# Kernel optimization log

Measured on AMD Instinct MI355X. Metric: run time of the kernel, lower is better.

## Reference

```python
import math
import jax, jax.numpy as jnp
import numpy as np

HALF_PI = math.pi / 2
TWOR_SCALE = 1.0 / math.log(2.0)
B, C, L, K = 32, 2, 262144, 4


def setup_inputs() -> dict:
    key = jax.random.key(0)
    ks = jax.random.split(key, 6)
    return {
        "input_signal": jax.random.normal(ks[0], (B, C, L), jnp.float32),
        "twoR": jax.random.normal(ks[1], (B, K), jnp.float32),
        "G": jax.random.normal(ks[2], (B, K), jnp.float32),
        "c_hp": jax.random.normal(ks[3], (B, K), jnp.float32),
        "c_bp": jax.random.normal(ks[4], (B, K), jnp.float32),
        "c_lp": jax.random.normal(ks[5], (B, K), jnp.float32),
    }


def get_biquad_coefficients(twoR, G, c_hp, c_bp, c_lp):
    # each arg: (B, K)
    G2 = G * G
    b0 = c_hp + c_bp * G + c_lp * G2
    b1 = -2.0 * c_hp + 2.0 * c_lp * G2
    b2 = c_hp - c_bp * G + c_lp * G2
    a0 = 1.0 + G2 + twoR * G
    a1 = 2.0 * G2 - 2.0
    a2 = 1.0 + G2 - twoR * G
    return jnp.stack([b0, b1, b2], -1), jnp.stack([a0, a1, a2], -1)  # (B,K,3)


def _biquad_cascade(x, Bs, As):
    # x: (B,C,L); Bs, As: (B,1,K,3) -- broadcast over channels.
    # Direct-form II transposed, cascaded in series over K filters.
    Bs = Bs / As[..., :1]
    As = As / As[..., :1]
    b_, c_ = x.shape[0], x.shape[1]
    y = x
    num_filters = Bs.shape[2]
    for k in range(num_filters):
        b0, b1, b2 = Bs[:, :, k, 0], Bs[:, :, k, 1], Bs[:, :, k, 2]  # (B,1)
        a1, a2 = As[:, :, k, 1], As[:, :, k, 2]  # (B,1)

        def step(carry, xt):
            s1, s2 = carry
            yt = b0 * xt + s1              # (B,C)
            s1n = b1 * xt - a1 * yt + s2
            s2n = b2 * xt - a2 * yt
            return (s1n, s2n), yt

        init = (jnp.zeros((b_, c_), y.dtype), jnp.zeros((b_, c_), y.dtype))
        _, yT = jax.lax.scan(step, init, jnp.moveaxis(y, -1, 0))  # (L,B,C)
        y = jnp.moveaxis(yT, 0, -1)
    return y


def reference(input_signal, twoR, G, c_hp, c_bp, c_lp):
    G = jnp.tan(HALF_PI * jax.nn.sigmoid(G))
    twoR = TWOR_SCALE * jax.nn.softplus(twoR) + 0.01
    Bs, As = get_biquad_coefficients(twoR, G, c_hp, c_bp, c_lp)  # (B,K,3)
    Bs, As = Bs[:, None], As[:, None]  # unsqueeze(1): (B,1,K,3)
    return _biquad_cascade(input_signal, Bs, As)
```

## Files before the change

### kernel.cpp

```cpp
#include <hip/hip_runtime.h>
#include <math.h>

#define B_N 32
#define C_N 2
#define L_N 262144
#define K_N 4
#define NSEQ (B_N * C_N)
#define CHUNK 32
#define THREADS 256
#define BLKSAMP (CHUNK * THREADS)
#define NBLK_SEQ (L_N / BLKSAMP)
#define NBLK_TOT (NSEQ * NBLK_SEQ)
#define NLVL 8
#define ROWW 33

#define WS_COEF 0
#define WS_PL   (B_N * 20)
#define WS_PBLK (WS_PL + B_N * NLVL * 64)
#define WS_AGG  (WS_PBLK + B_N * 64)

__global__ __launch_bounds__(64) void svf_prep(
    const float* __restrict__ twoR, const float* __restrict__ Graw,
    const float* __restrict__ c_hp, const float* __restrict__ c_bp,
    const float* __restrict__ c_lp, float* __restrict__ ws)
{
    const int b = blockIdx.x;
    const int t = threadIdx.x;
    __shared__ double cf[K_N][5];
    __shared__ double M[8][8];

    if (t < K_N) {
        const int k = t;
        double g  = (double)Graw[b * K_N + k];
        double tr = (double)twoR[b * K_N + k];
        double hp = (double)c_hp[b * K_N + k];
        double bp = (double)c_bp[b * K_N + k];
        double lp = (double)c_lp[b * K_N + k];
        double sg = 1.0 / (1.0 + exp(-g));
        double G  = tan(1.5707963267948966 * sg);
        double R  = log1p(exp(tr)) * 1.4426950408889634 + 0.01;
        double G2 = G * G;
        double b0 = hp + bp * G + lp * G2;
        double b1 = -2.0 * hp + 2.0 * lp * G2;
        double b2 = hp - bp * G + lp * G2;
        double a0 = 1.0 + G2 + R * G;
        double a1 = 2.0 * G2 - 2.0;
        double a2 = 1.0 + G2 - R * G;
        cf[k][0] = b0 / a0; cf[k][1] = b1 / a0; cf[k][2] = b2 / a0;
        cf[k][3] = a1 / a0; cf[k][4] = a2 / a0;
    }
    __syncthreads();

    if (t < 20) ws[WS_COEF + b * 20 + t] = (float)cf[t / 5][t % 5];

    if (t < 8) {
        double s[8];
        #pragma unroll
        for (int i = 0; i < 8; ++i) s[i] = (i == t) ? 1.0 : 0.0;
        double in = 0.0;
        #pragma unroll
        for (int k = 0; k < K_N; ++k) {
            double y   = cf[k][0] * in + s[2 * k];
            double s1n = cf[k][1] * in - cf[k][3] * y + s[2 * k + 1];
            double s2n = cf[k][2] * in - cf[k][4] * y;
            s[2 * k] = s1n; s[2 * k + 1] = s2n; in = y;
        }
        #pragma unroll
        for (int i = 0; i < 8; ++i) M[i][t] = s[i];
    }
    __syncthreads();

    const int i = t >> 3, j = t & 7;
    for (int p = 1; p <= 13; ++p) {
        double acc = 0.0;
        #pragma unroll
        for (int k = 0; k < 8; ++k) acc += M[i][k] * M[k][j];
        __syncthreads();
        M[i][j] = acc;
        __syncthreads();
        if (p >= 5 && p <= 12) ws[WS_PL + (b * NLVL + (p - 5)) * 64 + t] = (float)acc;
        if (p == 13)           ws[WS_PBLK + b * 64 + t] = (float)acc;
    }
}

__device__ __forceinline__ float cascade_step(const float cf[20], float s[8], float in)
{
    #pragma unroll
    for (int k = 0; k < K_N; ++k) {
        float y  = fmaf(cf[k * 5 + 0], in, s[2 * k]);
        float t1 = fmaf(cf[k * 5 + 1], in, s[2 * k + 1]);
        float n1 = fmaf(-cf[k * 5 + 3], y, t1);
        float n2 = fmaf(-cf[k * 5 + 4], y, cf[k * 5 + 2] * in);
        s[2 * k] = n1; s[2 * k + 1] = n2;
        in = y;
    }
    return in;
}

__device__ __forceinline__ void stage_load(const float4* __restrict__ xg4,
                                           float* __restrict__ win,
                                           float* __restrict__ xr, int tid)
{
    float4 v4[8];
    #pragma unroll
    for (int j = 0; j < 8; ++j) v4[j] = xg4[tid + j * THREADS];
    const int myw = tid >> 6, lane = tid & 63;
    #pragma unroll
    for (int r = 0; r < 4; ++r) {
        #pragma unroll
        for (int h = 0; h < 2; ++h) {
            const int fw = tid + h * THREADS;
            const int a  = (fw >> 3) * ROWW + (fw & 7) * 4;
            float4 v = v4[2 * r + h];
            win[a] = v.x; win[a + 1] = v.y; win[a + 2] = v.z; win[a + 3] = v.w;
        }
        __syncthreads();
        if (myw == r) {
            #pragma unroll
            for (int j = 0; j < CHUNK; ++j) xr[j] = win[lane * ROWW + j];
        }
        __syncthreads();
    }
}

__global__ __launch_bounds__(THREADS) void svf_pass1(
    const float* __restrict__ x, const float* __restrict__ ws,
    float* __restrict__ out)
{
    const int seq = blockIdx.x >> 5;
    const int blk = blockIdx.x & (NBLK_SEQ - 1);
    const int tid = threadIdx.x;
    const int b   = seq >> 1;

    __shared__ float smem[THREADS * 9];
    __shared__ float Pm[NLVL * 64];

    for (int q = tid; q < NLVL * 64; q += THREADS)
        Pm[q] = ws[WS_PL + b * NLVL * 64 + q];

    float cf[20];
    #pragma unroll
    for (int q = 0; q < 20; ++q) cf[q] = ws[WS_COEF + b * 20 + q];

    const size_t base = (size_t)seq * L_N + (size_t)blk * BLKSAMP;
    float xr[CHUNK];
    stage_load((const float4*)(x + base), smem, xr, tid);

    float t[8] = {0, 0, 0, 0, 0, 0, 0, 0};
    #pragma unroll
    for (int j = 0; j < CHUNK; ++j) (void)cascade_step(cf, t, xr[j]);

    for (int l = 0; l < NLVL; ++l) {
        const int d = 1 << l;
        #pragma unroll
        for (int q = 0; q < 8; ++q) smem[tid * 9 + q] = t[q];
        __syncthreads();
        float prev[8];
        const bool have = (tid >= d);
        if (have) {
            #pragma unroll
            for (int q = 0; q < 8; ++q) prev[q] = smem[(tid - d) * 9 + q];
        }
        __syncthreads();
        if (have) {
            #pragma unroll
            for (int r = 0; r < 8; ++r) {
                float acc = t[r];
                #pragma unroll
                for (int c = 0; c < 8; ++c)
                    acc = fmaf(Pm[l * 64 + r * 8 + c], prev[c], acc);
                t[r] = acc;
            }
        }
    }
    #pragma unroll
    for (int q = 0; q < 8; ++q) smem[tid * 9 + q] = t[q];
    __syncthreads();

    float e[8] = {0, 0, 0, 0, 0, 0, 0, 0};
    if (tid > 0) {
        #pragma unroll
        for (int q = 0; q < 8; ++q) e[q] = smem[(tid - 1) * 9 + q];
    }
    float4* eo = (float4*)(out + base);
    eo[2 * tid]     = make_float4(e[0], e[1], e[2], e[3]);
    eo[2 * tid + 1] = make_float4(e[4], e[5], e[6], e[7]);

    if (tid == THREADS - 1) {
        float* agg = (float*)ws + WS_AGG + (size_t)blockIdx.x * 8;
        #pragma unroll
        for (int q = 0; q < 8; ++q) agg[q] = t[q];
    }
}

__global__ __launch_bounds__(64) void svf_scanb(float* __restrict__ ws)
{
    const int seq = threadIdx.x;
    const int b   = seq >> 1;
    float P[64];
    #pragma unroll
    for (int q = 0; q < 64; ++q) P[q] = ws[WS_PBLK + b * 64 + q];

    float* agg = ws + WS_AGG + (size_t)seq * NBLK_SEQ * 8;

    float t[8] = {0, 0, 0, 0, 0, 0, 0, 0};
    for (int j = 0; j < NBLK_SEQ; ++j) {
        float f[8];
        #pragma unroll
        for (int q = 0; q < 8; ++q) f[q] = agg[j * 8 + q];
        #pragma unroll
        for (int q = 0; q < 8; ++q) agg[j * 8 + q] = t[q];
        float nt[8];
        #pragma unroll
        for (int r = 0; r < 8; ++r) {
            float acc = f[r];
            #pragma unroll
            for (int c = 0; c < 8; ++c) acc = fmaf(P[r * 8 + c], t[c], acc);
            nt[r] = acc;
        }
        #pragma unroll
        for (int q = 0; q < 8; ++q) t[q] = nt[q];
    }
}

__global__ __launch_bounds__(THREADS) void svf_pass2(
    const float* __restrict__ x, const float* __restrict__ ws,
    float* __restrict__ out)
{
    const int seq = blockIdx.x >> 5;
    const int blk = blockIdx.x & (NBLK_SEQ - 1);
    const int tid = threadIdx.x;
    const int b   = seq >> 1;

    __shared__ float smem[THREADS * 9];
    __shared__ float Pm[NLVL * 64];

    const size_t base = (size_t)seq * L_N + (size_t)blk * BLKSAMP;

    const float4* eo = (const float4*)(out + base);
    float4 e0 = eo[2 * tid], e1 = eo[2 * tid + 1];

    const float* sbp = ws + WS_AGG + (size_t)blockIdx.x * 8;
    float v[8];
    #pragma unroll
    for (int q = 0; q < 8; ++q) v[q] = sbp[q];

    for (int q = tid; q < NLVL * 64; q += THREADS)
        Pm[q] = ws[WS_PL + b * NLVL * 64 + q];

    float cf[20];
    #pragma unroll
    for (int q = 0; q < 20; ++q) cf[q] = ws[WS_COEF + b * 20 + q];

    float xr[CHUNK];
    stage_load((const float4*)(x + base), smem, xr, tid);

    #pragma unroll
    for (int l = 0; l < NLVL; ++l) {
        if ((tid >> l) & 1) {
            float nv[8];
            #pragma unroll
            for (int r = 0; r < 8; ++r) {
                float acc = 0.0f;
                #pragma unroll
                for (int c = 0; c < 8; ++c)
                    acc = fmaf(Pm[l * 64 + r * 8 + c], v[c], acc);
                nv[r] = acc;
            }
            #pragma unroll
            for (int q = 0; q < 8; ++q) v[q] = nv[q];
        }
    }

    float s[8] = {e0.x + v[0], e0.y + v[1], e0.z + v[2], e0.w + v[3],
                  e1.x + v[4], e1.y + v[5], e1.z + v[6], e1.w + v[7]};

    #pragma unroll
    for (int j = 0; j < CHUNK; ++j) xr[j] = cascade_step(cf, s, xr[j]);

    const int myw = tid >> 6, lane = tid & 63;
    float4* og4 = (float4*)(out + base);
    for (int r = 0; r < 4; ++r) {
        if (myw == r) {
            #pragma unroll
            for (int j = 0; j < CHUNK; ++j) smem[lane * ROWW + j] = xr[j];
        }
        __syncthreads();
        #pragma unroll
        for (int h = 0; h < 2; ++h) {
            const int fw = tid + h * THREADS;
            const int a  = (fw >> 3) * ROWW + (fw & 7) * 4;
            og4[r * 512 + fw] =
                make_float4(smem[a], smem[a + 1], smem[a + 2], smem[a + 3]);
        }
        __syncthreads();
    }
}

extern "C" void kernel_launch(void* const* d_in, const int* in_sizes, int n_in,
                              void* d_out, int out_size, void* d_ws, size_t ws_size,
                              hipStream_t stream)
{
    (void)in_sizes; (void)n_in; (void)out_size; (void)ws_size;
    const float* x    = (const float*)d_in[0];
    const float* twoR = (const float*)d_in[1];
    const float* G    = (const float*)d_in[2];
    const float* chp  = (const float*)d_in[3];
    const float* cbp  = (const float*)d_in[4];
    const float* clp  = (const float*)d_in[5];
    float* out = (float*)d_out;
    float* ws  = (float*)d_ws;

    svf_prep <<<B_N, 64, 0, stream>>>(twoR, G, chp, cbp, clp, ws);
    svf_pass1<<<NBLK_TOT, THREADS, 0, stream>>>(x, ws, out);
    svf_scanb<<<1, 64, 0, stream>>>(ws);
    svf_pass2<<<NBLK_TOT, THREADS, 0, stream>>>(x, ws, out);
}
```

Baseline: 163.9 us.

## Fuse two-pass scan into single kernel with decoupled lookback over flags

```diff
diff --git a/kernel.cpp b/kernel.cpp
--- a/kernel.cpp
+++ b/kernel.cpp
@@ -13,11 +13,12 @@
 #define NBLK_TOT (NSEQ * NBLK_SEQ)
 #define NLVL 8
 #define ROWW 33
+#define FLAG_READY 0x1F2E3D4Cu
 
 #define WS_COEF 0
 #define WS_PL   (B_N * 20)
-#define WS_PBLK (WS_PL + B_N * NLVL * 64)
-#define WS_AGG  (WS_PBLK + B_N * 64)
+#define WS_AGG  (WS_PL + B_N * NLVL * 64)
+#define WS_FLAG (WS_AGG + NBLK_TOT * 8)
 
 __global__ __launch_bounds__(64) void svf_prep(
     const float* __restrict__ twoR, const float* __restrict__ Graw,
@@ -26,6 +27,9 @@
 {
     const int b = blockIdx.x;
     const int t = threadIdx.x;
+
+    ((unsigned*)(ws + WS_FLAG))[b * 64 + t] = 0u;
+
     __shared__ double cf[K_N][5];
     __shared__ double M[8][8];
 
@@ -71,15 +75,14 @@
     __syncthreads();
 
     const int i = t >> 3, j = t & 7;
-    for (int p = 1; p <= 13; ++p) {
+    for (int p = 1; p <= 12; ++p) {
         double acc = 0.0;
         #pragma unroll
         for (int k = 0; k < 8; ++k) acc += M[i][k] * M[k][j];
         __syncthreads();
         M[i][j] = acc;
         __syncthreads();
-        if (p >= 5 && p <= 12) ws[WS_PL + (b * NLVL + (p - 5)) * 64 + t] = (float)acc;
-        if (p == 13)           ws[WS_PBLK + b * 64 + t] = (float)acc;
+        if (p >= 5) ws[WS_PL + (b * NLVL + (p - 5)) * 64 + t] = (float)acc;
     }
 }
 
@@ -97,14 +100,34 @@
     return in;
 }
 
-__device__ __forceinline__ void stage_load(const float4* __restrict__ xg4,
-                                           float* __restrict__ win,
-                                           float* __restrict__ xr, int tid)
-{
+__global__ __launch_bounds__(THREADS, 4) void svf_fused(
+    const float* __restrict__ x, float* __restrict__ ws, float* __restrict__ out)
+{
+    const int seq  = blockIdx.x >> 5;
+    const int blk  = blockIdx.x & (NBLK_SEQ - 1);
+    const int tid  = threadIdx.x;
+    const int b    = seq >> 1;
+    const int myw  = tid >> 6, lane = tid & 63;
+
+    __shared__ float smem[THREADS * 9];
+    __shared__ float Pm[NLVL * 64];
+    __shared__ float Pb[64];
+    __shared__ float fl[NBLK_SEQ][8];
+    __shared__ float sbv[8];
+
+    for (int q = tid; q < NLVL * 64; q += THREADS)
+        Pm[q] = ws[WS_PL + b * NLVL * 64 + q];
+
+    float cf[20];
+    #pragma unroll
+    for (int q = 0; q < 20; ++q) cf[q] = ws[WS_COEF + b * 20 + q];
+
+    const size_t base = (size_t)seq * L_N + (size_t)blk * BLKSAMP;
+    const float4* xg4 = (const float4*)(x + base);
     float4 v4[8];
     #pragma unroll
     for (int j = 0; j < 8; ++j) v4[j] = xg4[tid + j * THREADS];
-    const int myw = tid >> 6, lane = tid & 63;
+    float xr[CHUNK];
     #pragma unroll
     for (int r = 0; r < 4; ++r) {
         #pragma unroll
@@ -112,39 +135,24 @@
             const int fw = tid + h * THREADS;
             const int a  = (fw >> 3) * ROWW + (fw & 7) * 4;
             float4 v = v4[2 * r + h];
-            win[a] = v.x; win[a + 1] = v.y; win[a + 2] = v.z; win[a + 3] = v.w;
+            smem[a] = v.x; smem[a + 1] = v.y; smem[a + 2] = v.z; smem[a + 3] = v.w;
         }
         __syncthreads();
         if (myw == r) {
             #pragma unroll
-            for (int j = 0; j < CHUNK; ++j) xr[j] = win[lane * ROWW + j];
-        }
-        __syncthreads();
-    }
-}
-
-__global__ __launch_bounds__(THREADS) void svf_pass1(
-    const float* __restrict__ x, const float* __restrict__ ws,
-    float* __restrict__ out)
-{
-    const int seq = blockIdx.x >> 5;
-    const int blk = blockIdx.x & (NBLK_SEQ - 1);
-    const int tid = threadIdx.x;
-    const int b   = seq >> 1;
-
-    __shared__ float smem[THREADS * 9];
-    __shared__ float Pm[NLVL * 64];
-
-    for (int q = tid; q < NLVL * 64; q += THREADS)
-        Pm[q] = ws[WS_PL + b * NLVL * 64 + q];
-
-    float cf[20];
-    #pragma unroll
-    for (int q = 0; q < 20; ++q) cf[q] = ws[WS_COEF + b * 20 + q];
-
-    const size_t base = (size_t)seq * L_N + (size_t)blk * BLKSAMP;
-    float xr[CHUNK];
-    stage_load((const float4*)(x + base), smem, xr, tid);
+            for (int j = 0; j < CHUNK; ++j) xr[j] = smem[lane * ROWW + j];
+        }
+        __syncthreads();
+    }
+
+    if (tid < 64) {
+        const int r8 = tid >> 3, c8 = tid & 7;
+        float acc = 0.0f;
+        #pragma unroll
+        for (int k = 0; k < 8; ++k)
+            acc = fmaf(Pm[7 * 64 + r8 * 8 + k], Pm[7 * 64 + k * 8 + c8], acc);
+        Pb[tid] = acc;
+    }
 
     float t[8] = {0, 0, 0, 0, 0, 0, 0, 0};
     #pragma unroll
@@ -177,84 +185,48 @@
     for (int q = 0; q < 8; ++q) smem[tid * 9 + q] = t[q];
     __syncthreads();
 
-    float e[8] = {0, 0, 0, 0, 0, 0, 0, 0};
-    if (tid > 0) {
-        #pragma unroll
-        for (int q = 0; q < 8; ++q) e[q] = smem[(tid - 1) * 9 + q];
-    }
-    float4* eo = (float4*)(out + base);
-    eo[2 * tid]     = make_float4(e[0], e[1], e[2], e[3]);
-    eo[2 * tid + 1] = make_float4(e[4], e[5], e[6], e[7]);
-
+    float* aggp = ws + WS_AGG;
+    unsigned* flagp = (unsigned*)(ws + WS_FLAG);
     if (tid == THREADS - 1) {
-        float* agg = (float*)ws + WS_AGG + (size_t)blockIdx.x * 8;
-        #pragma unroll
-        for (int q = 0; q < 8; ++q) agg[q] = t[q];
-    }
-}
-
-__global__ __launch_bounds__(64) void svf_scanb(float* __restrict__ ws)
-{
-    const int seq = threadIdx.x;
-    const int b   = seq >> 1;
-    float P[64];
-    #pragma unroll
-    for (int q = 0; q < 64; ++q) P[q] = ws[WS_PBLK + b * 64 + q];
-
-    float* agg = ws + WS_AGG + (size_t)seq * NBLK_SEQ * 8;
-
-    float t[8] = {0, 0, 0, 0, 0, 0, 0, 0};
-    for (int j = 0; j < NBLK_SEQ; ++j) {
-        float f[8];
-        #pragma unroll
-        for (int q = 0; q < 8; ++q) f[q] = agg[j * 8 + q];
-        #pragma unroll
-        for (int q = 0; q < 8; ++q) agg[j * 8 + q] = t[q];
-        float nt[8];
-        #pragma unroll
-        for (int r = 0; r < 8; ++r) {
-            float acc = f[r];
-            #pragma unroll
-            for (int c = 0; c < 8; ++c) acc = fmaf(P[r * 8 + c], t[c], acc);
-            nt[r] = acc;
-        }
-        #pragma unroll
-        for (int q = 0; q < 8; ++q) t[q] = nt[q];
-    }
-}
-
-__global__ __launch_bounds__(THREADS) void svf_pass2(
-    const float* __restrict__ x, const float* __restrict__ ws,
-    float* __restrict__ out)
-{
-    const int seq = blockIdx.x >> 5;
-    const int blk = blockIdx.x & (NBLK_SEQ - 1);
-    const int tid = threadIdx.x;
-    const int b   = seq >> 1;
-
-    __shared__ float smem[THREADS * 9];
-    __shared__ float Pm[NLVL * 64];
-
-    const size_t base = (size_t)seq * L_N + (size_t)blk * BLKSAMP;
-
-    const float4* eo = (const float4*)(out + base);
-    float4 e0 = eo[2 * tid], e1 = eo[2 * tid + 1];
-
-    const float* sbp = ws + WS_AGG + (size_t)blockIdx.x * 8;
+        #pragma unroll
+        for (int q = 0; q < 8; ++q)
+            __hip_atomic_store(&aggp[(size_t)blockIdx.x * 8 + q], t[q],
+                               __ATOMIC_RELAXED, __HIP_MEMORY_SCOPE_AGENT);
+        __threadfence();
+        __hip_atomic_store(&flagp[blockIdx.x], FLAG_READY,
+                           __ATOMIC_RELEASE, __HIP_MEMORY_SCOPE_AGENT);
+    }
+
+    if (tid < 64) {
+        if (lane < blk) {
+            const int pj = (seq << 5) + lane;
+            while (__hip_atomic_load(&flagp[pj], __ATOMIC_ACQUIRE,
+                                     __HIP_MEMORY_SCOPE_AGENT) != FLAG_READY)
+                __builtin_amdgcn_s_sleep(2);
+            #pragma unroll
+            for (int q = 0; q < 8; ++q)
+                fl[lane][q] = __hip_atomic_load(&aggp[(size_t)pj * 8 + q],
+                                                __ATOMIC_RELAXED, __HIP_MEMORY_SCOPE_AGENT);
+        }
+        if (lane < 8) {
+            float tr_ = 0.0f;
+            for (int j = 0; j < blk; ++j) {
+                float tc[8];
+                #pragma unroll
+                for (int c = 0; c < 8; ++c) tc[c] = __shfl(tr_, c);
+                float acc = fl[j][lane];
+                #pragma unroll
+                for (int c = 0; c < 8; ++c) acc = fmaf(Pb[lane * 8 + c], tc[c], acc);
+                tr_ = acc;
+            }
+            sbv[lane] = tr_;
+        }
+    }
+    __syncthreads();
+
     float v[8];
     #pragma unroll
-    for (int q = 0; q < 8; ++q) v[q] = sbp[q];
-
-    for (int q = tid; q < NLVL * 64; q += THREADS)
-        Pm[q] = ws[WS_PL + b * NLVL * 64 + q];
-
-    float cf[20];
-    #pragma unroll
-    for (int q = 0; q < 20; ++q) cf[q] = ws[WS_COEF + b * 20 + q];
-
-    float xr[CHUNK];
-    stage_load((const float4*)(x + base), smem, xr, tid);
-
+    for (int q = 0; q < 8; ++q) v[q] = sbv[q];
     #pragma unroll
     for (int l = 0; l < NLVL; ++l) {
         if ((tid >> l) & 1) {
@@ -272,13 +244,19 @@
         }
     }
 
-    float s[8] = {e0.x + v[0], e0.y + v[1], e0.z + v[2], e0.w + v[3],
-                  e1.x + v[4], e1.y + v[5], e1.z + v[6], e1.w + v[7]};
+    float s[8];
+    if (tid == 0) {
+        #pragma unroll
+        for (int q = 0; q < 8; ++q) s[q] = v[q];
+    } else {
+        #pragma unroll
+        for (int q = 0; q < 8; ++q) s[q] = smem[(tid - 1) * 9 + q] + v[q];
+    }
+    __syncthreads();
 
     #pragma unroll
     for (int j = 0; j < CHUNK; ++j) xr[j] = cascade_step(cf, s, xr[j]);
 
-    const int myw = tid >> 6, lane = tid & 63;
     float4* og4 = (float4*)(out + base);
     for (int r = 0; r < 4; ++r) {
         if (myw == r) {
@@ -312,7 +290,5 @@
     float* ws  = (float*)d_ws;
 
     svf_prep <<<B_N, 64, 0, stream>>>(twoR, G, chp, cbp, clp, ws);
-    svf_pass1<<<NBLK_TOT, THREADS, 0, stream>>>(x, ws, out);
-    svf_scanb<<<1, 64, 0, stream>>>(ws);
-    svf_pass2<<<NBLK_TOT, THREADS, 0, stream>>>(x, ws, out);
-}
+    svf_fused<<<NBLK_TOT, THREADS, 0, stream>>>(x, ws, out);
+}
```

After: 304.1 us. 85.6% more time.
